# Optimization experiments

Hardware: AMD Instinct MI355X
Metric: run time of the kernel (lower is better)

## Reference

```python
import jax, jax.numpy as jnp
import numpy as np

B, C, H, W = 16, 3, 512, 512
NUM_BANDS = 100


def setup_inputs() -> dict:
    key = jax.random.key(0)
    k1, k2, k3 = jax.random.split(key, 3)
    clean = jax.random.normal(k1, (B, C, H, W), dtype=jnp.float32)
    noisy = jax.random.normal(k2, (B, C, H, W), dtype=jnp.float32)
    # value_prob = arange(1.0, 0.0, -0.01) * 0.3, bernoulli per batch row
    probs = (1.0 - 0.01 * jnp.arange(NUM_BANDS, dtype=jnp.float32)) * 0.3  # (100,)
    value_set = jax.random.bernoulli(k3, probs[None, :].repeat(B, axis=0)).astype(jnp.float32)  # (B,100)
    return {"clean": clean, "noisy": noisy, "value_set": value_set}


def reference(clean, noisy, value_set):
    b, c, h, w = noisy.shape
    # radial distance map from image center (meshgrid 'ij' as in torch)
    a = jnp.arange(h, dtype=jnp.float32)[:, None]
    bb = jnp.arange(w, dtype=jnp.float32)[None, :]
    dist = jnp.sqrt((a - h / 2) ** 2 + (bb - w / 2) ** 2)  # (H,W)
    max_radius = float(np.sqrt(h * h + w * w) / 2)
    radius_set = max_radius * jnp.arange(0.01, 1.01, 0.01, dtype=jnp.float32)  # (100,)

    # FFT + full fftshift (torch default shifts ALL axes, incl. batch/channel)
    noisy_fq = jnp.fft.fftshift(jnp.fft.fftn(noisy, axes=(-1, -2)))
    clean_fq = jnp.fft.fftshift(jnp.fft.fftn(clean, axes=(-1, -2)))

    # Fused bucketize + gather replacing the 100-iteration mask loop:
    # band i covers radius_set[i-1] <= dist < radius_set[i]  ->  searchsorted right
    idx = jnp.searchsorted(radius_set, dist, side='right')  # (H,W), values in [0,100]
    in_range = idx < radius_set.shape[0]
    idx_c = jnp.minimum(idx, radius_set.shape[0] - 1)
    bn1_mask = jnp.where(in_range[None, :, :], value_set[:, idx_c], 0.0)  # (B,H,W)
    bn2_mask = 1.0 - bn1_mask

    replaced_fq = noisy_fq * bn1_mask[:, None, :, :] + clean_fq * bn2_mask[:, None, :, :]
    replaced_fq = jnp.fft.ifftshift(replaced_fq)
    out = jnp.fft.ifftn(replaced_fq, axes=(-1, -2))
    return out.real
```

## Files before the change

### kernel.cpp

```cpp
#include <hip/hip_runtime.h>
#include <math.h>


using cplx = float2;

__device__ __forceinline__ cplx cmul(cplx a, cplx b){
  return make_float2(a.x*b.x - a.y*b.y, a.x*b.y + a.y*b.x);
}
__device__ __forceinline__ cplx cadd(cplx a, cplx b){ return make_float2(a.x+b.x, a.y+b.y); }
__device__ __forceinline__ cplx csub(cplx a, cplx b){ return make_float2(a.x-b.x, a.y-b.y); }
template<int S> __device__ __forceinline__ cplx muli(cplx a){
  return (S < 0) ? make_float2(a.y, -a.x) : make_float2(-a.y, a.x);
}
__device__ __forceinline__ int sw(int i){ return i ^ (((i >> 6) & 7) << 1); }

template<int S>
__device__ __forceinline__ void dft8(cplx v[8]){
  const float R2 = 0.70710678118654752440f;
  cplx e0 = cadd(v[0], v[4]), e1 = csub(v[0], v[4]);
  cplx o0 = cadd(v[2], v[6]), o1 = muli<S>(csub(v[2], v[6]));
  cplx E0 = cadd(e0, o0), E1 = cadd(e1, o1), E2 = csub(e0, o0), E3 = csub(e1, o1);
  cplx f0 = cadd(v[1], v[5]), f1 = csub(v[1], v[5]);
  cplx g0 = cadd(v[3], v[7]), g1 = muli<S>(csub(v[3], v[7]));
  cplx F0 = cadd(f0, g0), F1 = cadd(f1, g1), F2 = csub(f0, g0), F3 = csub(f1, g1);
  const cplx w1 = make_float2( R2, (float)S * R2);
  const cplx w3 = make_float2(-R2, (float)S * R2);
  cplx t0 = F0, t1 = cmul(w1, F1), t2 = muli<S>(F2), t3 = cmul(w3, F3);
  v[0] = cadd(E0, t0); v[4] = csub(E0, t0);
  v[1] = cadd(E1, t1); v[5] = csub(E1, t1);
  v[2] = cadd(E2, t2); v[6] = csub(E2, t2);
  v[3] = cadd(E3, t3); v[7] = csub(E3, t3);
}

__device__ __forceinline__ void twiddle8(cplx v[8], float ang){
  float sn, cs; __sincosf(ang, &sn, &cs);
  cplx w = make_float2(cs, sn), cur = w;
  #pragma unroll
  for(int r = 1; r < 8; r++){ v[r] = cmul(v[r], cur); cur = cmul(cur, w); }
}

template<int S>
__device__ __forceinline__ void fft512(cplx v[8], cplx* s, int t){
  const float PI2 = 6.283185307179586f;
  dft8<S>(v);
  #pragma unroll
  for(int r = 0; r < 8; r++) s[sw(t*8 + r)] = v[r];
  #pragma unroll
  for(int r = 0; r < 8; r++) v[r] = s[sw(t + 64*r)];
  twiddle8(v, (float)S * PI2 * (1.0f/64.0f) * (float)(t & 7));
  dft8<S>(v);
  int d1 = ((t >> 3) << 6) | (t & 7);
  #pragma unroll
  for(int r = 0; r < 8; r++) s[sw(d1 + (r << 3))] = v[r];
  #pragma unroll
  for(int r = 0; r < 8; r++) v[r] = s[sw(t + 64*r)];
  twiddle8(v, (float)S * PI2 * (1.0f/512.0f) * (float)t);
  dft8<S>(v);
}

__global__ __launch_bounds__(256) void k_rowfft(const float* __restrict__ noisy,
                                                const float* __restrict__ clean,
                                                float2* __restrict__ ws){
  __shared__ cplx sbuf[4][512];
  int wid = threadIdx.x >> 6, t = threadIdx.x & 63;
  size_t row = (size_t)blockIdx.x * 4 + wid;
  const float* np_ = noisy + row * 512;
  const float* cp_ = clean + row * 512;
  cplx v[8];
  #pragma unroll
  for(int r = 0; r < 8; r++){ int i = t + 64*r; v[r] = make_float2(np_[i] - cp_[i], 0.0f); }
  fft512<-1>(v, sbuf[wid], t);
  float2* op = ws + row * 512;
  #pragma unroll
  for(int r = 0; r < 8; r++) op[t + 64*r] = v[r];
}

#define INV_BAND 0.27621358640099513f

__global__ __launch_bounds__(256) void k_colfft(float2* __restrict__ ws,
                                                const float* __restrict__ value_set){
  __shared__ cplx tile[512][9];
  __shared__ cplx scr[4][512];
  int img = blockIdx.x >> 6;
  int w0  = (blockIdx.x & 63) << 3;
  int b   = img / 3;
  const float* vs = value_set + ((b + 8) & 15) * 100;
  float2* base = ws + (size_t)img * (512 * 512);

  #pragma unroll
  for(int h0 = 0; h0 < 512; h0 += 32){
    int h = h0 + (threadIdx.x >> 3), j = threadIdx.x & 7;
    tile[h][j] = base[(size_t)h * 512 + w0 + j];
  }
  __syncthreads();

  int wid = threadIdx.x >> 6, t = threadIdx.x & 63;
  #pragma unroll 1
  for(int jj = 0; jj < 2; jj++){
    int j = (wid << 1) | jj;
    int w = w0 + j;
    int fw = (w < 256) ? w : w - 512;
    int fw2 = fw * fw;
    cplx v[8];
    #pragma unroll
    for(int r = 0; r < 8; r++) v[r] = tile[t + 64*r][j];
    fft512<-1>(v, scr[wid], t);
    #pragma unroll
    for(int r = 0; r < 8; r++){
      int h = t + 64*r;
      int fh = (h < 256) ? h : h - 512;
      float rr = sqrtf((float)(fh*fh + fw2));
      int idx = (int)(rr * INV_BAND);
      float sel = (idx < 100) ? vs[idx] : 0.0f;
      float sc = sel * (1.0f / 262144.0f);
      v[r].x *= sc; v[r].y *= sc;
    }
    fft512<1>(v, scr[wid], t);
    #pragma unroll
    for(int r = 0; r < 8; r++) tile[t + 64*r][j] = v[r];
  }
  __syncthreads();

  #pragma unroll
  for(int h0 = 0; h0 < 512; h0 += 32){
    int h = h0 + (threadIdx.x >> 3), j = threadIdx.x & 7;
    base[(size_t)h * 512 + w0 + j] = tile[h][j];
  }
}

__global__ __launch_bounds__(256) void k_rowifft(const float2* __restrict__ ws,
                                                 const float* __restrict__ clean,
                                                 float* __restrict__ out){
  __shared__ cplx sbuf[4][512];
  int wid = threadIdx.x >> 6, t = threadIdx.x & 63;
  size_t row = (size_t)blockIdx.x * 4 + wid;
  const float2* ip = ws + row * 512;
  cplx v[8];
  #pragma unroll
  for(int r = 0; r < 8; r++) v[r] = ip[t + 64*r];
  fft512<1>(v, sbuf[wid], t);
  const float* cp_ = clean + row * 512;
  float* op = out + row * 512;
  #pragma unroll
  for(int r = 0; r < 8; r++) op[t + 64*r] = v[r].x + cp_[t + 64*r];
}

extern "C" void kernel_launch(void* const* d_in, const int* in_sizes, int n_in,
                              void* d_out, int out_size, void* d_ws, size_t ws_size,
                              hipStream_t stream){
  const float* clean     = (const float*)d_in[0];
  const float* noisy     = (const float*)d_in[1];
  const float* value_set = (const float*)d_in[2];
  float* out = (float*)d_out;
  float2* ws = (float2*)d_ws;

  k_rowfft <<<6144, 256, 0, stream>>>(noisy, clean, ws);
  k_colfft <<<3072, 256, 0, stream>>>(ws, value_set);
  k_rowifft<<<6144, 256, 0, stream>>>(ws, clean, out);
}
```

Measured before the change: 256.6 us.

## Pack two real images per complex FFT and split spectra via conjugate symmetry

```diff
diff --git a/kernel.cpp b/kernel.cpp
--- a/kernel.cpp
+++ b/kernel.cpp
@@ -32,47 +32,71 @@
   v[3] = cadd(E3, t3); v[7] = csub(E3, t3);
 }
 
-__device__ __forceinline__ void twiddle8(cplx v[8], float ang){
-  float sn, cs; __sincosf(ang, &sn, &cs);
-  cplx w = make_float2(cs, sn), cur = w;
-  #pragma unroll
-  for(int r = 1; r < 8; r++){ v[r] = cmul(v[r], cur); cur = cmul(cur, w); }
-}
-
 template<int S>
-__device__ __forceinline__ void fft512(cplx v[8], cplx* s, int t){
+__device__ __forceinline__ void twiddle8_pair(cplx a[8], cplx b[8], float ang){
+  float sn, c_; __sincosf(ang, &sn, &c_);
+  cplx w = make_float2(c_, sn), cur = w;
+  #pragma unroll
+  for(int r = 1; r < 8; r++){ a[r] = cmul(a[r], cur); b[r] = cmul(b[r], cur); cur = cmul(cur, w); }
+}
+
+template<int S, int STR>
+__device__ __forceinline__ void fft512_pair(cplx a[8], cplx b[8], cplx* sa, cplx* sb, int t){
   const float PI2 = 6.283185307179586f;
-  dft8<S>(v);
-  #pragma unroll
-  for(int r = 0; r < 8; r++) s[sw(t*8 + r)] = v[r];
-  #pragma unroll
-  for(int r = 0; r < 8; r++) v[r] = s[sw(t + 64*r)];
-  twiddle8(v, (float)S * PI2 * (1.0f/64.0f) * (float)(t & 7));
-  dft8<S>(v);
+  dft8<S>(a); dft8<S>(b);
+  #pragma unroll
+  for(int r = 0; r < 8; r++){ int i = sw(t*8 + r)*STR; sa[i] = a[r]; sb[i] = b[r]; }
+  #pragma unroll
+  for(int r = 0; r < 8; r++){ int i = sw(t + 64*r)*STR; a[r] = sa[i]; b[r] = sb[i]; }
+  twiddle8_pair<S>(a, b, (float)S * PI2 * (1.0f/64.0f) * (float)(t & 7));
+  dft8<S>(a); dft8<S>(b);
   int d1 = ((t >> 3) << 6) | (t & 7);
   #pragma unroll
-  for(int r = 0; r < 8; r++) s[sw(d1 + (r << 3))] = v[r];
-  #pragma unroll
-  for(int r = 0; r < 8; r++) v[r] = s[sw(t + 64*r)];
-  twiddle8(v, (float)S * PI2 * (1.0f/512.0f) * (float)t);
-  dft8<S>(v);
+  for(int r = 0; r < 8; r++){ int i = sw(d1 + (r << 3))*STR; sa[i] = a[r]; sb[i] = b[r]; }
+  #pragma unroll
+  for(int r = 0; r < 8; r++){ int i = sw(t + 64*r)*STR; a[r] = sa[i]; b[r] = sb[i]; }
+  twiddle8_pair<S>(a, b, (float)S * PI2 * (1.0f/512.0f) * (float)t);
+  dft8<S>(a); dft8<S>(b);
+}
+
+__device__ __forceinline__ void packed_images(int p, int& i0, int& i1, int& b1, int& b2){
+  if (p < 16){ i0 = 3*p; i1 = 3*p + 1; b1 = p; b2 = p; }
+  else { int q = p - 16; i0 = 6*q + 2; i1 = 6*q + 5; b1 = 2*q; b2 = 2*q + 1; }
+}
+
+__device__ __forceinline__ int slot_col(int s, int j){
+  int c = (j < 4) ? (4*s + j) : (505 - 4*s + j);
+  c &= 511;
+  if (s == 0 && j == 7) c = 256;
+  return c;
 }
 
 __global__ __launch_bounds__(256) void k_rowfft(const float* __restrict__ noisy,
                                                 const float* __restrict__ clean,
                                                 float2* __restrict__ ws){
-  __shared__ cplx sbuf[4][512];
+  __shared__ cplx scr[8][512];
+  int blk = blockIdx.x;
+  int p = blk >> 6, h8 = (blk & 63) << 3;
+  int i0, i1, b1, b2; packed_images(p, i0, i1, b1, b2);
+  const float* n0 = noisy + (size_t)i0 * 262144;
+  const float* c0 = clean + (size_t)i0 * 262144;
+  const float* n1 = noisy + (size_t)i1 * 262144;
+  const float* c1 = clean + (size_t)i1 * 262144;
   int wid = threadIdx.x >> 6, t = threadIdx.x & 63;
-  size_t row = (size_t)blockIdx.x * 4 + wid;
-  const float* np_ = noisy + row * 512;
-  const float* cp_ = clean + row * 512;
-  cplx v[8];
-  #pragma unroll
-  for(int r = 0; r < 8; r++){ int i = t + 64*r; v[r] = make_float2(np_[i] - cp_[i], 0.0f); }
-  fft512<-1>(v, sbuf[wid], t);
-  float2* op = ws + row * 512;
-  #pragma unroll
-  for(int r = 0; r < 8; r++) op[t + 64*r] = v[r];
+  int hA = h8 + wid*2, hB = hA + 1;
+  cplx a[8], b[8];
+  #pragma unroll
+  for(int r = 0; r < 8; r++){
+    int iA = hA*512 + t + 64*r;
+    int iB = hB*512 + t + 64*r;
+    a[r] = make_float2(n0[iA]-c0[iA], n1[iA]-c1[iA]);
+    b[r] = make_float2(n0[iB]-c0[iB], n1[iB]-c1[iB]);
+  }
+  fft512_pair<-1,1>(a, b, scr[wid*2], scr[wid*2+1], t);
+  float2* oA = ws + (size_t)p*262144 + hA*512;
+  float2* oB = ws + (size_t)p*262144 + hB*512;
+  #pragma unroll
+  for(int r = 0; r < 8; r++){ oA[t+64*r] = a[r]; oB[t+64*r] = b[r]; }
 }
 
 #define INV_BAND 0.27621358640099513f
@@ -80,69 +104,109 @@
 __global__ __launch_bounds__(256) void k_colfft(float2* __restrict__ ws,
                                                 const float* __restrict__ value_set){
   __shared__ cplx tile[512][9];
-  __shared__ cplx scr[4][512];
-  int img = blockIdx.x >> 6;
-  int w0  = (blockIdx.x & 63) << 3;
-  int b   = img / 3;
-  const float* vs = value_set + ((b + 8) & 15) * 100;
-  float2* base = ws + (size_t)img * (512 * 512);
-
-  #pragma unroll
-  for(int h0 = 0; h0 < 512; h0 += 32){
-    int h = h0 + (threadIdx.x >> 3), j = threadIdx.x & 7;
-    tile[h][j] = base[(size_t)h * 512 + w0 + j];
+  int blk = blockIdx.x;
+  int p = blk >> 6, s = blk & 63;
+  int i0, i1, b1, b2; packed_images(p, i0, i1, b1, b2);
+  const float* vs1 = value_set + ((b1 + 8) & 15) * 100;
+  const float* vs2 = value_set + ((b2 + 8) & 15) * 100;
+  float2* base = ws + (size_t)p * 262144;
+  int tid = threadIdx.x;
+
+  {
+    int j = tid & 7, cj = slot_col(s, j);
+    #pragma unroll
+    for(int h0 = 0; h0 < 512; h0 += 32){
+      int h = h0 + (tid >> 3);
+      tile[h][j] = base[h*512 + cj];
+    }
   }
   __syncthreads();
 
-  int wid = threadIdx.x >> 6, t = threadIdx.x & 63;
-  #pragma unroll 1
-  for(int jj = 0; jj < 2; jj++){
-    int j = (wid << 1) | jj;
-    int w = w0 + j;
-    int fw = (w < 256) ? w : w - 512;
-    int fw2 = fw * fw;
-    cplx v[8];
+  int wid = tid >> 6, t = tid & 63;
+  int sA = wid, sB = 7 - wid;
+  int colA = slot_col(s, sA);
+  int colB = slot_col(s, sB);
+  int fwA = (colA < 256) ? colA : colA - 512;
+  int fwB = (colB < 256) ? colB : colB - 512;
+  int fw2A = fwA * fwA;
+  int fw2B = fwB * fwB;
+  bool selfp = (s == 0 && wid == 0);
+  int pA = selfp ? sA : sB;
+  int pB = selfp ? sB : sA;
+
+  cplx a[8], b[8];
+  #pragma unroll
+  for(int r = 0; r < 8; r++){ a[r] = tile[t+64*r][sA]; b[r] = tile[t+64*r][sB]; }
+  fft512_pair<-1,9>(a, b, &tile[0][sA], &tile[0][sB], t);
+  #pragma unroll
+  for(int r = 0; r < 8; r++){ tile[t+64*r][sA] = a[r]; tile[t+64*r][sB] = b[r]; }
+  #pragma unroll
+  for(int r = 0; r < 8; r++){
+    int h = t + 64*r;
+    int fh = (h < 256) ? h : h - 512;
+    int fh2 = fh * fh;
+    float rrA = sqrtf((float)(fh2 + fw2A));
+    float rrB = sqrtf((float)(fh2 + fw2B));
+    int bandA = (int)(rrA * INV_BAND);
+    int bandB = (int)(rrB * INV_BAND);
+    float m1A = (bandA < 100) ? vs1[bandA] : 0.0f;
+    float m2A = (bandA < 100) ? vs2[bandA] : 0.0f;
+    float m1B = (bandB < 100) ? vs1[bandB] : 0.0f;
+    float m2B = (bandB < 100) ? vs2[bandB] : 0.0f;
+    float csA = 0.5f*(m1A + m2A) * (1.0f/262144.0f);
+    float cdA = 0.5f*(m1A - m2A) * (1.0f/262144.0f);
+    float csB = 0.5f*(m1B + m2B) * (1.0f/262144.0f);
+    float cdB = 0.5f*(m1B - m2B) * (1.0f/262144.0f);
+    int ph = (512 - h) & 511;
+    float2 PA = tile[ph][pA];
+    float2 PB = tile[ph][pB];
+    cplx na = make_float2(csA*a[r].x + cdA*PA.x, csA*a[r].y - cdA*PA.y);
+    cplx nb = make_float2(csB*b[r].x + cdB*PB.x, csB*b[r].y - cdB*PB.y);
+    a[r] = na; b[r] = nb;
+  }
+  fft512_pair<1,9>(a, b, &tile[0][sA], &tile[0][sB], t);
+  #pragma unroll
+  for(int r = 0; r < 8; r++){ tile[t+64*r][sA] = a[r]; tile[t+64*r][sB] = b[r]; }
+  __syncthreads();
+
+  {
+    int j = tid & 7, cj = slot_col(s, j);
     #pragma unroll
-    for(int r = 0; r < 8; r++) v[r] = tile[t + 64*r][j];
-    fft512<-1>(v, scr[wid], t);
-    #pragma unroll
-    for(int r = 0; r < 8; r++){
-      int h = t + 64*r;
-      int fh = (h < 256) ? h : h - 512;
-      float rr = sqrtf((float)(fh*fh + fw2));
-      int idx = (int)(rr * INV_BAND);
-      float sel = (idx < 100) ? vs[idx] : 0.0f;
-      float sc = sel * (1.0f / 262144.0f);
-      v[r].x *= sc; v[r].y *= sc;
+    for(int h0 = 0; h0 < 512; h0 += 32){
+      int h = h0 + (tid >> 3);
+      base[h*512 + cj] = tile[h][j];
     }
-    fft512<1>(v, scr[wid], t);
-    #pragma unroll
-    for(int r = 0; r < 8; r++) tile[t + 64*r][j] = v[r];
-  }
-  __syncthreads();
-
-  #pragma unroll
-  for(int h0 = 0; h0 < 512; h0 += 32){
-    int h = h0 + (threadIdx.x >> 3), j = threadIdx.x & 7;
-    base[(size_t)h * 512 + w0 + j] = tile[h][j];
   }
 }
 
 __global__ __launch_bounds__(256) void k_rowifft(const float2* __restrict__ ws,
                                                  const float* __restrict__ clean,
                                                  float* __restrict__ out){
-  __shared__ cplx sbuf[4][512];
+  __shared__ cplx scr[8][512];
+  int blk = blockIdx.x;
+  int p = blk >> 6, h8 = (blk & 63) << 3;
+  int i0, i1, b1, b2; packed_images(p, i0, i1, b1, b2);
   int wid = threadIdx.x >> 6, t = threadIdx.x & 63;
-  size_t row = (size_t)blockIdx.x * 4 + wid;
-  const float2* ip = ws + row * 512;
-  cplx v[8];
-  #pragma unroll
-  for(int r = 0; r < 8; r++) v[r] = ip[t + 64*r];
-  fft512<1>(v, sbuf[wid], t);
-  const float* cp_ = clean + row * 512;
-  float* op = out + row * 512;
-  #pragma unroll
-  for(int r = 0; r < 8; r++) op[t + 64*r] = v[r].x + cp_[t + 64*r];
+  int hA = h8 + wid*2, hB = hA + 1;
+  const float2* iA_ = ws + (size_t)p*262144 + hA*512;
+  const float2* iB_ = ws + (size_t)p*262144 + hB*512;
+  cplx a[8], b[8];
+  #pragma unroll
+  for(int r = 0; r < 8; r++){ a[r] = iA_[t+64*r]; b[r] = iB_[t+64*r]; }
+  fft512_pair<1,1>(a, b, scr[wid*2], scr[wid*2+1], t);
+  const float* c0 = clean + (size_t)i0 * 262144;
+  const float* c1 = clean + (size_t)i1 * 262144;
+  float* o0 = out + (size_t)i0 * 262144;
+  float* o1 = out + (size_t)i1 * 262144;
+  #pragma unroll
+  for(int r = 0; r < 8; r++){
+    int iA = hA*512 + t + 64*r;
+    int iB = hB*512 + t + 64*r;
+    o0[iA] = a[r].x + c0[iA];
+    o1[iA] = a[r].y + c1[iA];
+    o0[iB] = b[r].x + c0[iB];
+    o1[iB] = b[r].y + c1[iB];
+  }
 }
 
 extern "C" void kernel_launch(void* const* d_in, const int* in_sizes, int n_in,
@@ -154,7 +218,7 @@
   float* out = (float*)d_out;
   float2* ws = (float2*)d_ws;
 
-  k_rowfft <<<6144, 256, 0, stream>>>(noisy, clean, ws);
-  k_colfft <<<3072, 256, 0, stream>>>(ws, value_set);
-  k_rowifft<<<6144, 256, 0, stream>>>(ws, clean, out);
-}
+  k_rowfft <<<1536, 256, 0, stream>>>(noisy, clean, ws);
+  k_colfft <<<1536, 256, 0, stream>>>(ws, value_set);
+  k_rowifft<<<1536, 256, 0, stream>>>(ws, clean, out);
+}
```

Measured after the change: 227.8 us. -11.2%, faster.
